# Performance work log

Measured on AMD Instinct MI355X. Metric: run time of the kernel, lower is better.

Reference implementation:

```python
import jax, jax.numpy as jnp
import numpy as np

# Block sizes (DGL message-flow-graph / sampled blocks)
NS0, ND0, NE0 = 300000, 50000, 800000   # block0: 2-hop frontier -> 1-hop frontier
NS1, ND1, NE1 = 50000, 8192, 131072     # block1: 1-hop frontier -> seed nodes


def _graph_conv(x, src, dst, ew, W, b, n_src, n_dst, weight_first):
    """DGL GraphConv with norm='both' and edge_weight.

    x: [n_src, d_in] source-node features; (src, dst): edge endpoints;
    ew: [E] edge weights. Degrees are UNWEIGHTED (copy of DGL semantics),
    clamped to >= 1. Weight applied before aggregation iff d_in > d_out.
    """
    ones_e = jnp.ones_like(ew)
    out_deg = jnp.clip(jax.ops.segment_sum(ones_e, src, num_segments=n_src), 1.0, None)
    h = x * (out_deg ** -0.5)[:, None]
    if weight_first:
        h = h @ W
    # gather-weight-scatter: m_v = sum_{e: e->v} ew_e * h_{src_e}
    msg = jax.ops.segment_sum(ew[:, None] * h[src], dst, num_segments=n_dst)
    in_deg = jnp.clip(jax.ops.segment_sum(ones_e, dst, num_segments=n_dst), 1.0, None)
    msg = msg * (in_deg ** -0.5)[:, None]
    if not weight_first:
        msg = msg @ W
    return msg + b


def setup_inputs() -> dict:
    key = jax.random.key(0)
    ks = jax.random.split(key, 12)
    in_f, hid_f, out_f = 256, 128, 128
    return {
        "x": jax.random.normal(ks[0], (NS0, in_f), dtype=jnp.float32),
        "src0": jax.random.randint(ks[1], (NE0,), 0, NS0, dtype=jnp.int64 if jax.config.jax_enable_x64 else jnp.int32).astype(jnp.int32),
        "dst0": jax.random.randint(ks[2], (NE0,), 0, ND0).astype(jnp.int32),
        "ew0": jax.random.normal(ks[3], (NE0,), dtype=jnp.float32),
        "src1": jax.random.randint(ks[4], (NE1,), 0, NS1).astype(jnp.int32),
        "dst1": jax.random.randint(ks[5], (NE1,), 0, ND1).astype(jnp.int32),
        "ew1": jax.random.normal(ks[6], (NE1,), dtype=jnp.float32),
        "W1": jax.random.normal(ks[7], (in_f, hid_f), dtype=jnp.float32) * 0.05,
        "b1": jax.random.normal(ks[8], (hid_f,), dtype=jnp.float32) * 0.05,
        "W2": jax.random.normal(ks[9], (hid_f, out_f), dtype=jnp.float32) * 0.05,
        "b2": jax.random.normal(ks[10], (out_f,), dtype=jnp.float32) * 0.05,
    }


def reference(x, src0, dst0, ew0, src1, dst1, ew1, W1, b1, W2, b2):
    # layer 1: in(256) > hidden(128) -> weight applied before aggregation
    h = jax.nn.relu(_graph_conv(x, src0, dst0, ew0, W1, b1, NS0, ND0, weight_first=True))
    # layer 2: hidden(128) <= out(128) -> aggregate then weight
    out = jax.nn.relu(_graph_conv(h, src1, dst1, ew1, W2, b2, NS1, ND1, weight_first=False))
    return out  # [ND1, out_f]
```

## Files before the change

### kernel.cpp

```cpp
#include <hip/hip_runtime.h>

#define NS0 300000
#define ND0 50000
#define NE0 800000
#define NS1 50000
#define ND1 8192
#define NE1 131072
#define IN_F 256
#define HID_F 128
#define SLOTS 64

#define OFF_OUTDEG0I 0
#define OFF_OUTDEG1I 300000
#define OFF_CNT0     350000
#define OFF_CNT1     400000
#define ZERO_WORDS   408192
#define OFF_EDGE0    408192
#define OFF_EDGE1    6808192
#define OFF_H1       7856768

__global__ __launch_bounds__(256) void k_zero(int4* __restrict__ p, int n4) {
  int i = blockIdx.x * 256 + threadIdx.x;
  int s = gridDim.x * 256;
  for (; i < n4; i += s) p[i] = make_int4(0, 0, 0, 0);
}

__global__ __launch_bounds__(256) void k_hist(
    const int* __restrict__ src0, const int* __restrict__ src1,
    int* __restrict__ outdeg0, int* __restrict__ outdeg1) {
  int tid = blockIdx.x * blockDim.x + threadIdx.x;
  int stride = gridDim.x * blockDim.x;
  for (int i = tid; i < NE0; i += stride) atomicAdd(&outdeg0[src0[i]], 1);
  for (int i = tid; i < NE1; i += stride) atomicAdd(&outdeg1[src1[i]], 1);
}

__global__ __launch_bounds__(256) void k_scatter(
    const int* __restrict__ src0, const int* __restrict__ dst0,
    const float* __restrict__ ew0, const int* __restrict__ outdeg0,
    int* __restrict__ cnt0, int2* __restrict__ edge0,
    const int* __restrict__ src1, const int* __restrict__ dst1,
    const float* __restrict__ ew1, const int* __restrict__ outdeg1,
    int* __restrict__ cnt1, int2* __restrict__ edge1) {
  int tid = blockIdx.x * blockDim.x + threadIdx.x;
  int stride = gridDim.x * blockDim.x;
  for (int i = tid; i < NE0; i += stride) {
    int s = src0[i];
    int d = dst0[i];
    float c = ew0[i] * rsqrtf(fmaxf((float)outdeg0[s], 1.0f));
    int slot = atomicAdd(&cnt0[d], 1);
    if (slot < SLOTS) edge0[d * SLOTS + slot] = make_int2(s, __float_as_int(c));
  }
  for (int i = tid; i < NE1; i += stride) {
    int s = src1[i];
    int d = dst1[i];
    float c = ew1[i] * rsqrtf(fmaxf((float)outdeg1[s], 1.0f));
    int slot = atomicAdd(&cnt1[d], 1);
    if (slot < SLOTS) edge1[d * SLOTS + slot] = make_int2(s, __float_as_int(c));
  }
}

#define FMA4(acc, c, v)                          \
  acc.x = fmaf(c, v.x, acc.x);                   \
  acc.y = fmaf(c, v.y, acc.y);                   \
  acc.z = fmaf(c, v.z, acc.z);                   \
  acc.w = fmaf(c, v.w, acc.w);

__global__ __launch_bounds__(256) void k_layer1(
    const float* __restrict__ x, const int* __restrict__ cnt,
    const int2* __restrict__ edge, const float* __restrict__ W1,
    const float* __restrict__ b1, float* __restrict__ h1) {
  __shared__ float arow[8][IN_F];
  const int t = blockIdx.x;
  const int wv = threadIdx.x >> 6;
  const int lane = threadIdx.x & 63;

#pragma unroll
  for (int rr = 0; rr < 2; ++rr) {
    const int row = t * 8 + wv * 2 + rr;
    const int deg = min(cnt[row], SLOTS);
    const int2* ep = edge + (size_t)row * SLOTS;
    float4 acc = make_float4(0.f, 0.f, 0.f, 0.f);
    int e = 0;
    for (; e + 8 <= deg; e += 8) {
      int2 p0 = ep[e + 0], p1 = ep[e + 1], p2 = ep[e + 2], p3 = ep[e + 3];
      int2 p4 = ep[e + 4], p5 = ep[e + 5], p6 = ep[e + 6], p7 = ep[e + 7];
      float4 v0 = *reinterpret_cast<const float4*>(x + (size_t)p0.x * IN_F + lane * 4);
      float4 v1 = *reinterpret_cast<const float4*>(x + (size_t)p1.x * IN_F + lane * 4);
      float4 v2 = *reinterpret_cast<const float4*>(x + (size_t)p2.x * IN_F + lane * 4);
      float4 v3 = *reinterpret_cast<const float4*>(x + (size_t)p3.x * IN_F + lane * 4);
      float4 v4 = *reinterpret_cast<const float4*>(x + (size_t)p4.x * IN_F + lane * 4);
      float4 v5 = *reinterpret_cast<const float4*>(x + (size_t)p5.x * IN_F + lane * 4);
      float4 v6 = *reinterpret_cast<const float4*>(x + (size_t)p6.x * IN_F + lane * 4);
      float4 v7 = *reinterpret_cast<const float4*>(x + (size_t)p7.x * IN_F + lane * 4);
      FMA4(acc, __int_as_float(p0.y), v0);
      FMA4(acc, __int_as_float(p1.y), v1);
      FMA4(acc, __int_as_float(p2.y), v2);
      FMA4(acc, __int_as_float(p3.y), v3);
      FMA4(acc, __int_as_float(p4.y), v4);
      FMA4(acc, __int_as_float(p5.y), v5);
      FMA4(acc, __int_as_float(p6.y), v6);
      FMA4(acc, __int_as_float(p7.y), v7);
    }
    for (; e + 2 <= deg; e += 2) {
      int2 pA = ep[e], pB = ep[e + 1];
      float4 vA = *reinterpret_cast<const float4*>(x + (size_t)pA.x * IN_F + lane * 4);
      float4 vB = *reinterpret_cast<const float4*>(x + (size_t)pB.x * IN_F + lane * 4);
      FMA4(acc, __int_as_float(pA.y), vA);
      FMA4(acc, __int_as_float(pB.y), vB);
    }
    if (e < deg) {
      int2 p = ep[e];
      float4 v = *reinterpret_cast<const float4*>(x + (size_t)p.x * IN_F + lane * 4);
      FMA4(acc, __int_as_float(p.y), v);
    }
    const float sc = rsqrtf(fmaxf((float)deg, 1.0f));
    *reinterpret_cast<float4*>(&arow[wv * 2 + rr][lane * 4]) =
        make_float4(acc.x * sc, acc.y * sc, acc.z * sc, acc.w * sc);
  }
  __syncthreads();

  const int j = threadIdx.x & 127;
  const int rg = threadIdx.x >> 7;
  float a0 = 0.f, a1 = 0.f, a2 = 0.f, a3 = 0.f;
  const float* wj = W1 + j;
#pragma unroll 8
  for (int k = 0; k < IN_F; ++k) {
    const float wvv = wj[(size_t)k * 128];
    a0 = fmaf(arow[rg * 4 + 0][k], wvv, a0);
    a1 = fmaf(arow[rg * 4 + 1][k], wvv, a1);
    a2 = fmaf(arow[rg * 4 + 2][k], wvv, a2);
    a3 = fmaf(arow[rg * 4 + 3][k], wvv, a3);
  }
  const float bj = b1[j];
  const int row0 = t * 8 + rg * 4;
  h1[(size_t)(row0 + 0) * 128 + j] = fmaxf(a0 + bj, 0.0f);
  h1[(size_t)(row0 + 1) * 128 + j] = fmaxf(a1 + bj, 0.0f);
  h1[(size_t)(row0 + 2) * 128 + j] = fmaxf(a2 + bj, 0.0f);
  h1[(size_t)(row0 + 3) * 128 + j] = fmaxf(a3 + bj, 0.0f);
}

#define FMA2(acc, c, v)                          \
  acc.x = fmaf(c, v.x, acc.x);                   \
  acc.y = fmaf(c, v.y, acc.y);

__global__ __launch_bounds__(256) void k_layer2(
    const float* __restrict__ h1, const int* __restrict__ cnt,
    const int2* __restrict__ edge, const float* __restrict__ W2,
    const float* __restrict__ b2, float* __restrict__ out) {
  __shared__ float arow[8][HID_F];
  const int t = blockIdx.x;
  const int wv = threadIdx.x >> 6;
  const int lane = threadIdx.x & 63;

#pragma unroll
  for (int rr = 0; rr < 2; ++rr) {
    const int row = t * 8 + wv * 2 + rr;
    const int deg = min(cnt[row], SLOTS);
    const int2* ep = edge + (size_t)row * SLOTS;
    float2 acc = make_float2(0.f, 0.f);
    int e = 0;
    for (; e + 4 <= deg; e += 4) {
      int2 p0 = ep[e + 0], p1 = ep[e + 1], p2 = ep[e + 2], p3 = ep[e + 3];
      float2 v0 = *reinterpret_cast<const float2*>(h1 + (size_t)p0.x * HID_F + lane * 2);
      float2 v1 = *reinterpret_cast<const float2*>(h1 + (size_t)p1.x * HID_F + lane * 2);
      float2 v2 = *reinterpret_cast<const float2*>(h1 + (size_t)p2.x * HID_F + lane * 2);
      float2 v3 = *reinterpret_cast<const float2*>(h1 + (size_t)p3.x * HID_F + lane * 2);
      FMA2(acc, __int_as_float(p0.y), v0);
      FMA2(acc, __int_as_float(p1.y), v1);
      FMA2(acc, __int_as_float(p2.y), v2);
      FMA2(acc, __int_as_float(p3.y), v3);
    }
    for (; e < deg; ++e) {
      int2 p = ep[e];
      float2 v = *reinterpret_cast<const float2*>(h1 + (size_t)p.x * HID_F + lane * 2);
      FMA2(acc, __int_as_float(p.y), v);
    }
    const float sc = rsqrtf(fmaxf((float)deg, 1.0f));
    *reinterpret_cast<float2*>(&arow[wv * 2 + rr][lane * 2]) =
        make_float2(acc.x * sc, acc.y * sc);
  }
  __syncthreads();

  const int j = threadIdx.x & 127;
  const int rg = threadIdx.x >> 7;
  float a0 = 0.f, a1 = 0.f, a2 = 0.f, a3 = 0.f;
  const float* wj = W2 + j;
#pragma unroll 8
  for (int k = 0; k < HID_F; ++k) {
    const float wvv = wj[(size_t)k * 128];
    a0 = fmaf(arow[rg * 4 + 0][k], wvv, a0);
    a1 = fmaf(arow[rg * 4 + 1][k], wvv, a1);
    a2 = fmaf(arow[rg * 4 + 2][k], wvv, a2);
    a3 = fmaf(arow[rg * 4 + 3][k], wvv, a3);
  }
  const float bj = b2[j];
  const int row0 = t * 8 + rg * 4;
  out[(size_t)(row0 + 0) * 128 + j] = fmaxf(a0 + bj, 0.0f);
  out[(size_t)(row0 + 1) * 128 + j] = fmaxf(a1 + bj, 0.0f);
  out[(size_t)(row0 + 2) * 128 + j] = fmaxf(a2 + bj, 0.0f);
  out[(size_t)(row0 + 3) * 128 + j] = fmaxf(a3 + bj, 0.0f);
}

extern "C" void kernel_launch(void* const* d_in, const int* in_sizes, int n_in,
                              void* d_out, int out_size, void* d_ws, size_t ws_size,
                              hipStream_t stream) {
  const float* x    = (const float*)d_in[0];
  const int*   src0 = (const int*)d_in[1];
  const int*   dst0 = (const int*)d_in[2];
  const float* ew0  = (const float*)d_in[3];
  const int*   src1 = (const int*)d_in[4];
  const int*   dst1 = (const int*)d_in[5];
  const float* ew1  = (const float*)d_in[6];
  const float* W1   = (const float*)d_in[7];
  const float* b1   = (const float*)d_in[8];
  const float* W2   = (const float*)d_in[9];
  const float* b2   = (const float*)d_in[10];
  float* out = (float*)d_out;

  int*   wsi = (int*)d_ws;
  float* wsf = (float*)d_ws;
  int* outdeg0 = wsi + OFF_OUTDEG0I;
  int* outdeg1 = wsi + OFF_OUTDEG1I;
  int* cnt0    = wsi + OFF_CNT0;
  int* cnt1    = wsi + OFF_CNT1;
  int2* edge0  = (int2*)(wsi + OFF_EDGE0);
  int2* edge1  = (int2*)(wsi + OFF_EDGE1);
  float* h1    = wsf + OFF_H1;

  k_zero<<<128, 256, 0, stream>>>((int4*)d_ws, ZERO_WORDS / 4);
  k_hist<<<512, 256, 0, stream>>>(src0, src1, outdeg0, outdeg1);
  k_scatter<<<2048, 256, 0, stream>>>(src0, dst0, ew0, outdeg0, cnt0, edge0,
                                      src1, dst1, ew1, outdeg1, cnt1, edge1);
  k_layer1<<<ND0 / 8, 256, 0, stream>>>(x, cnt0, edge0, W1, b1, h1);
  k_layer2<<<ND1 / 8, 256, 0, stream>>>(h1, cnt1, edge1, W2, b2, out);
}
```

Baseline: 282.9 us.

## Split layer-1 gather into two feature-half passes to shrink random-access working set

The layer-1 aggregation is split into two kernels. The first gathers only the low 128 features of each source row into a workspace buffer. The second gathers the high 128 features, reloads the stored low half into shared memory, and runs the matmul. The aim is to halve the working set touched by each random-gather pass so more of x stays cache-resident, at the cost of an extra kernel launch, a second read of the edge lists, and an extra write and read of a 50000x128 intermediate.

New measurement: 313.9 us. +10.9%, slower.

```diff
diff --git a/kernel.cpp b/kernel.cpp
--- a/kernel.cpp
+++ b/kernel.cpp
@@ -18,6 +18,7 @@
 #define OFF_EDGE0    408192
 #define OFF_EDGE1    6808192
 #define OFF_H1       7856768
+#define OFF_AGGLO    14256768
 
 __global__ __launch_bounds__(256) void k_zero(int4* __restrict__ p, int n4) {
   int i = blockIdx.x * 256 + threadIdx.x;
@@ -59,63 +60,90 @@
   }
 }
 
-#define FMA4(acc, c, v)                          \
-  acc.x = fmaf(c, v.x, acc.x);                   \
-  acc.y = fmaf(c, v.y, acc.y);                   \
-  acc.z = fmaf(c, v.z, acc.z);                   \
-  acc.w = fmaf(c, v.w, acc.w);
-
-__global__ __launch_bounds__(256) void k_layer1(
+#define FMA2(acc, c, v)        \
+  acc.x = fmaf(c, v.x, acc.x); \
+  acc.y = fmaf(c, v.y, acc.y);
+
+__global__ __launch_bounds__(256) void k_gather_lo(
     const float* __restrict__ x, const int* __restrict__ cnt,
-    const int2* __restrict__ edge, const float* __restrict__ W1,
-    const float* __restrict__ b1, float* __restrict__ h1) {
-  __shared__ float arow[8][IN_F];
+    const int2* __restrict__ edge, float* __restrict__ agg_lo) {
   const int t = blockIdx.x;
   const int wv = threadIdx.x >> 6;
   const int lane = threadIdx.x & 63;
-
 #pragma unroll
   for (int rr = 0; rr < 2; ++rr) {
     const int row = t * 8 + wv * 2 + rr;
     const int deg = min(cnt[row], SLOTS);
     const int2* ep = edge + (size_t)row * SLOTS;
-    float4 acc = make_float4(0.f, 0.f, 0.f, 0.f);
+    float2 acc = make_float2(0.f, 0.f);
     int e = 0;
-    for (; e + 8 <= deg; e += 8) {
+    for (; e + 4 <= deg; e += 4) {
       int2 p0 = ep[e + 0], p1 = ep[e + 1], p2 = ep[e + 2], p3 = ep[e + 3];
-      int2 p4 = ep[e + 4], p5 = ep[e + 5], p6 = ep[e + 6], p7 = ep[e + 7];
-      float4 v0 = *reinterpret_cast<const float4*>(x + (size_t)p0.x * IN_F + lane * 4);
-      float4 v1 = *reinterpret_cast<const float4*>(x + (size_t)p1.x * IN_F + lane * 4);
-      float4 v2 = *reinterpret_cast<const float4*>(x + (size_t)p2.x * IN_F + lane * 4);
-      float4 v3 = *reinterpret_cast<const float4*>(x + (size_t)p3.x * IN_F + lane * 4);
-      float4 v4 = *reinterpret_cast<const float4*>(x + (size_t)p4.x * IN_F + lane * 4);
-      float4 v5 = *reinterpret_cast<const float4*>(x + (size_t)p5.x * IN_F + lane * 4);
-      float4 v6 = *reinterpret_cast<const float4*>(x + (size_t)p6.x * IN_F + lane * 4);
-      float4 v7 = *reinterpret_cast<const float4*>(x + (size_t)p7.x * IN_F + lane * 4);
-      FMA4(acc, __int_as_float(p0.y), v0);
-      FMA4(acc, __int_as_float(p1.y), v1);
-      FMA4(acc, __int_as_float(p2.y), v2);
-      FMA4(acc, __int_as_float(p3.y), v3);
-      FMA4(acc, __int_as_float(p4.y), v4);
-      FMA4(acc, __int_as_float(p5.y), v5);
-      FMA4(acc, __int_as_float(p6.y), v6);
-      FMA4(acc, __int_as_float(p7.y), v7);
-    }
-    for (; e + 2 <= deg; e += 2) {
-      int2 pA = ep[e], pB = ep[e + 1];
-      float4 vA = *reinterpret_cast<const float4*>(x + (size_t)pA.x * IN_F + lane * 4);
-      float4 vB = *reinterpret_cast<const float4*>(x + (size_t)pB.x * IN_F + lane * 4);
-      FMA4(acc, __int_as_float(pA.y), vA);
-      FMA4(acc, __int_as_float(pB.y), vB);
-    }
-    if (e < deg) {
+      float2 v0 = *reinterpret_cast<const float2*>(x + (size_t)p0.x * IN_F + lane * 2);
+      float2 v1 = *reinterpret_cast<const float2*>(x + (size_t)p1.x * IN_F + lane * 2);
+      float2 v2 = *reinterpret_cast<const float2*>(x + (size_t)p2.x * IN_F + lane * 2);
+      float2 v3 = *reinterpret_cast<const float2*>(x + (size_t)p3.x * IN_F + lane * 2);
+      FMA2(acc, __int_as_float(p0.y), v0);
+      FMA2(acc, __int_as_float(p1.y), v1);
+      FMA2(acc, __int_as_float(p2.y), v2);
+      FMA2(acc, __int_as_float(p3.y), v3);
+    }
+    for (; e < deg; ++e) {
       int2 p = ep[e];
-      float4 v = *reinterpret_cast<const float4*>(x + (size_t)p.x * IN_F + lane * 4);
-      FMA4(acc, __int_as_float(p.y), v);
+      float2 v = *reinterpret_cast<const float2*>(x + (size_t)p.x * IN_F + lane * 2);
+      FMA2(acc, __int_as_float(p.y), v);
     }
     const float sc = rsqrtf(fmaxf((float)deg, 1.0f));
-    *reinterpret_cast<float4*>(&arow[wv * 2 + rr][lane * 4]) =
-        make_float4(acc.x * sc, acc.y * sc, acc.z * sc, acc.w * sc);
+    *reinterpret_cast<float2*>(agg_lo + (size_t)row * 128 + lane * 2) =
+        make_float2(acc.x * sc, acc.y * sc);
+  }
+}
+
+__global__ __launch_bounds__(256) void k_layer1b(
+    const float* __restrict__ x, const int* __restrict__ cnt,
+    const int2* __restrict__ edge, const float* __restrict__ agg_lo,
+    const float* __restrict__ W1, const float* __restrict__ b1,
+    float* __restrict__ h1) {
+  __shared__ float arow[8][IN_F];
+  const int t = blockIdx.x;
+  const int wv = threadIdx.x >> 6;
+  const int lane = threadIdx.x & 63;
+
+  {
+    const float4* srcv = reinterpret_cast<const float4*>(agg_lo + (size_t)t * 8 * 128);
+    const int i = threadIdx.x;
+    float4 v = srcv[i];
+    const int r = i >> 5;
+    const int c4 = i & 31;
+    *reinterpret_cast<float4*>(&arow[r][c4 * 4]) = v;
+  }
+
+#pragma unroll
+  for (int rr = 0; rr < 2; ++rr) {
+    const int row = t * 8 + wv * 2 + rr;
+    const int deg = min(cnt[row], SLOTS);
+    const int2* ep = edge + (size_t)row * SLOTS;
+    float2 acc = make_float2(0.f, 0.f);
+    int e = 0;
+    for (; e + 4 <= deg; e += 4) {
+      int2 p0 = ep[e + 0], p1 = ep[e + 1], p2 = ep[e + 2], p3 = ep[e + 3];
+      float2 v0 = *reinterpret_cast<const float2*>(x + (size_t)p0.x * IN_F + 128 + lane * 2);
+      float2 v1 = *reinterpret_cast<const float2*>(x + (size_t)p1.x * IN_F + 128 + lane * 2);
+      float2 v2 = *reinterpret_cast<const float2*>(x + (size_t)p2.x * IN_F + 128 + lane * 2);
+      float2 v3 = *reinterpret_cast<const float2*>(x + (size_t)p3.x * IN_F + 128 + lane * 2);
+      FMA2(acc, __int_as_float(p0.y), v0);
+      FMA2(acc, __int_as_float(p1.y), v1);
+      FMA2(acc, __int_as_float(p2.y), v2);
+      FMA2(acc, __int_as_float(p3.y), v3);
+    }
+    for (; e < deg; ++e) {
+      int2 p = ep[e];
+      float2 v = *reinterpret_cast<const float2*>(x + (size_t)p.x * IN_F + 128 + lane * 2);
+      FMA2(acc, __int_as_float(p.y), v);
+    }
+    const float sc = rsqrtf(fmaxf((float)deg, 1.0f));
+    *reinterpret_cast<float2*>(&arow[wv * 2 + rr][128 + lane * 2]) =
+        make_float2(acc.x * sc, acc.y * sc);
   }
   __syncthreads();
 
@@ -138,10 +166,6 @@
   h1[(size_t)(row0 + 2) * 128 + j] = fmaxf(a2 + bj, 0.0f);
   h1[(size_t)(row0 + 3) * 128 + j] = fmaxf(a3 + bj, 0.0f);
 }
-
-#define FMA2(acc, c, v)                          \
-  acc.x = fmaf(c, v.x, acc.x);                   \
-  acc.y = fmaf(c, v.y, acc.y);
 
 __global__ __launch_bounds__(256) void k_layer2(
     const float* __restrict__ h1, const int* __restrict__ cnt,
@@ -226,11 +250,13 @@
   int2* edge0  = (int2*)(wsi + OFF_EDGE0);
   int2* edge1  = (int2*)(wsi + OFF_EDGE1);
   float* h1    = wsf + OFF_H1;
+  float* agglo = wsf + OFF_AGGLO;
 
   k_zero<<<128, 256, 0, stream>>>((int4*)d_ws, ZERO_WORDS / 4);
   k_hist<<<512, 256, 0, stream>>>(src0, src1, outdeg0, outdeg1);
   k_scatter<<<2048, 256, 0, stream>>>(src0, dst0, ew0, outdeg0, cnt0, edge0,
                                       src1, dst1, ew1, outdeg1, cnt1, edge1);
-  k_layer1<<<ND0 / 8, 256, 0, stream>>>(x, cnt0, edge0, W1, b1, h1);
+  k_gather_lo<<<ND0 / 8, 256, 0, stream>>>(x, cnt0, edge0, agglo);
+  k_layer1b<<<ND0 / 8, 256, 0, stream>>>(x, cnt0, edge0, agglo, W1, b1, h1);
   k_layer2<<<ND1 / 8, 256, 0, stream>>>(h1, cnt1, edge1, W2, b2, out);
 }
```
